# Kernel optimization log

Hardware: AMD Instinct MI355X
Metric: run time of the kernel (lower is better)

The kernel has to match this reference:

```python
import math
import jax, jax.numpy as jnp
import numpy as np

N, D, H, K = 200000, 512, 256, 64  # stocks, input_size, hidden_size, latent_size (heads)


def setup_inputs() -> dict:
    key = jax.random.key(0)
    ks = jax.random.split(key, 11)
    s = 0.02  # weight init scale
    return {
        "e": jax.random.normal(ks[0], (N, D), dtype=jnp.float32),
        "q": jax.random.normal(ks[1], (K, H), dtype=jnp.float32),  # learnable query per head
        "Wk": jax.random.normal(ks[2], (K, H, D), dtype=jnp.float32) * s,
        "bk": jax.random.normal(ks[3], (K, H), dtype=jnp.float32) * s,
        "Wv": jax.random.normal(ks[4], (K, H, D), dtype=jnp.float32) * s,
        "bv": jax.random.normal(ks[5], (K, H), dtype=jnp.float32) * s,
        "mu_w": jax.random.normal(ks[6], (H,), dtype=jnp.float32) * s,
        "mu_b": jax.random.normal(ks[7], (), dtype=jnp.float32) * s,
        "sigma_w": jax.random.normal(ks[8], (H,), dtype=jnp.float32) * s,
        "sigma_b": jax.random.normal(ks[9], (), dtype=jnp.float32) * s,
    }


def reference(e, q, Wk, bk, Wv, bv, mu_w, mu_b, sigma_w, sigma_b):
    # Per head k: scores = q . (Wk @ e_i + bk) / sqrt(H)   -> [K, N]
    # Computed as (q @ Wk) @ e.T + q.bk, avoiding the [K, N, H] key tensor.
    scale = 1.0 / math.sqrt(H)
    qWk = jnp.einsum('kh,khd->kd', q, Wk)                      # [K, D]
    scores = (jnp.einsum('kd,nd->kn', qWk, e)
              + jnp.einsum('kh,kh->k', q, bk)[:, None]) * scale  # [K, N]
    attn = jax.nn.softmax(scores, axis=-1)                     # softmax over stocks
    # h_att = attn @ (e @ Wv.T + bv); since attn sums to 1, bias term is bv exactly.
    pooled = jnp.einsum('kn,nd->kd', attn, e)                  # [K, D]
    h_multi = jnp.einsum('kd,khd->kh', pooled, Wv) + bv        # [K, H]
    mu_prior = h_multi @ mu_w + mu_b                           # [K]
    sigma_prior = jnp.exp(h_multi @ sigma_w + sigma_b)         # [K]
    return mu_prior, sigma_prior
```

## Files before the change

kernel.cpp:

```cpp
#include <hip/hip_runtime.h>
#include <math.h>
#include <stdint.h>

#define NROWS 200000
#define DDIM  512
#define HDIM  256
#define KHEADS 64
#define NB    32
#define NITER (NROWS / NB)
#define GRID  512

typedef __attribute__((ext_vector_type(8))) short bf16x8;
typedef __attribute__((ext_vector_type(4))) float f32x4;

__device__ __forceinline__ uint32_t f2bf1(float x) {
    uint32_t u = __float_as_uint(x);
    return (u + 0x7FFFu + ((u >> 16) & 1u)) >> 16;
}
__device__ __forceinline__ uint32_t pk2(float a, float b) {
    uint32_t r;
    asm("v_cvt_pk_bf16_f32 %0, %1, %2" : "=v"(r) : "v"(a), "v"(b));
    return r;
}

__global__ __launch_bounds__(256)
void prep(const float* __restrict__ q, const float* __restrict__ Wk,
          unsigned short* __restrict__ qwkb)
{
    const int k    = blockIdx.x >> 3;
    const int dq   = blockIdx.x & 7;
    const int t    = threadIdx.x;
    const int cd   = t & 63;
    const int hseg = t >> 6;
    const int d    = dq * 64 + cd;
    const float* wk = Wk + ((size_t)k << 17);
    const float* qk = q + (k << 8);
    const float* wp = wk + (hseg * 64) * 512 + d;
    const float* qp = qk + hseg * 64;
    float s0 = 0.f, s1 = 0.f, s2 = 0.f, s3 = 0.f;
    #pragma unroll 4
    for (int h = 0; h < 64; h += 4) {
        s0 = fmaf(qp[h],     wp[(h    ) * 512], s0);
        s1 = fmaf(qp[h + 1], wp[(h + 1) * 512], s1);
        s2 = fmaf(qp[h + 2], wp[(h + 2) * 512], s2);
        s3 = fmaf(qp[h + 3], wp[(h + 3) * 512], s3);
    }
    float s = (s0 + s1) + (s2 + s3);
    __shared__ float red[4][64];
    red[hseg][cd] = s;
    __syncthreads();
    if (t < 64) {
        float tot = (red[0][t] + red[1][t]) + (red[2][t] + red[3][t]);
        qwkb[(k << 9) + dq * 64 + t] = (unsigned short)f2bf1(tot * 0.0625f);
    }
}

__global__ void qbk_kernel(const float* __restrict__ q, const float* __restrict__ bk,
                           float* __restrict__ qbk)
{
    int k = threadIdx.x;
    const float4* q4 = (const float4*)(q + (k << 8));
    const float4* b4 = (const float4*)(bk + (k << 8));
    float s = 0.f;
    for (int i = 0; i < 64; ++i) {
        float4 a = q4[i], b = b4[i];
        s += a.x * b.x + a.y * b.y + a.z * b.z + a.w * b.w;
    }
    qbk[k] = s * 0.0625f;
}

__global__ __launch_bounds__(256, 2)
void fused_attn(const float* __restrict__ e,
                const unsigned short* __restrict__ qwkb,
                const float* __restrict__ qbk,
                float* __restrict__ pooled, float* __restrict__ lsum,
                float* __restrict__ parts, float* __restrict__ lparts,
                int use_parts)
{
    __shared__ char lds[65536];

    const int t    = threadIdx.x;
    const int w    = t >> 6;
    const int lane = t & 63;
    const int c    = lane & 15;
    const int Q    = lane >> 4;

    bf16x8 bq[16];
    {
        const char* qb_ = (const char*)qwkb + (w * 16 + c) * 1024 + Q * 16;
        #pragma unroll
        for (int ks = 0; ks < 16; ++ks)
            bq[ks] = *(const bf16x8*)(qb_ + ks * 64);
    }
    const float qbias = qbk[w * 16 + c];

    f32x4 acc[32];
    #pragma unroll
    for (int i = 0; i < 32; ++i) { f32x4 z = {0.f, 0.f, 0.f, 0.f}; acc[i] = z; }
    float l_part = 0.f;

    for (int b = blockIdx.x; b < NITER; b += GRID) {
        __syncthreads();
        const float4* eg = (const float4*)(e + (size_t)b * (NB * DDIM));
        #pragma unroll
        for (int i = 0; i < 4; ++i) {
            const int bb = t + i * 256;
            const int rg = bb >> 7, dg = bb & 127;
            float4 v0 = eg[(rg * 4 + 0) * 128 + dg];
            float4 v1 = eg[(rg * 4 + 1) * 128 + dg];
            float4 v2 = eg[(rg * 4 + 2) * 128 + dg];
            float4 v3 = eg[(rg * 4 + 3) * 128 + dg];
            const float* r0 = (const float*)&v0;
            const float* r1 = (const float*)&v1;
            const float* r2 = (const float*)&v2;
            const float* r3 = (const float*)&v3;
            {
                const int chA  = (rg >> 2) * 16 + (dg >> 3);
                const int lnD  = ((dg >> 1) & 3) * 16;
                const int byA  = (dg & 1) * 8;
                const int base = chA * 1024 + byA;
                const int sw   = chA & 7;
                int ln0 = (((rg & 3) * 4 + 0) + lnD) ^ sw;
                int ln1 = (((rg & 3) * 4 + 1) + lnD) ^ sw;
                int ln2 = (((rg & 3) * 4 + 2) + lnD) ^ sw;
                int ln3 = (((rg & 3) * 4 + 3) + lnD) ^ sw;
                *(uint2*)(lds + base + ln0 * 16) = make_uint2(pk2(r0[0], r0[1]), pk2(r0[2], r0[3]));
                *(uint2*)(lds + base + ln1 * 16) = make_uint2(pk2(r1[0], r1[1]), pk2(r1[2], r1[3]));
                *(uint2*)(lds + base + ln2 * 16) = make_uint2(pk2(r2[0], r2[1]), pk2(r2[2], r2[3]));
                *(uint2*)(lds + base + ln3 * 16) = make_uint2(pk2(r3[0], r3[1]), pk2(r3[2], r3[3]));
            }
            {
                const int chB  = dg >> 2;
                const int lnR  = ((rg >> 1) & 3) * 16;
                const int byB  = (rg & 1) * 8;
                const int base = 32768 + chB * 1024 + byB;
                const int sw   = chB & 7;
                #pragma unroll
                for (int i3 = 0; i3 < 4; ++i3) {
                    int ln = (((dg & 3) * 4 + i3) + lnR) ^ sw;
                    *(uint2*)(lds + base + ln * 16) =
                        make_uint2(pk2(r0[i3], r1[i3]), pk2(r2[i3], r3[i3]));
                }
            }
        }
        __syncthreads();

        f32x4 c10 = {0.f, 0.f, 0.f, 0.f};
        f32x4 c11 = {0.f, 0.f, 0.f, 0.f};
        #pragma unroll
        for (int ks = 0; ks < 16; ++ks) {
            const bf16x8 a0 = *(const bf16x8*)(lds + ks * 1024        + ((lane ^ (ks & 7)) * 16));
            const bf16x8 a1 = *(const bf16x8*)(lds + (16 + ks) * 1024 + ((lane ^ ((16 + ks) & 7)) * 16));
            c10 = __builtin_amdgcn_mfma_f32_16x16x32_bf16(a0, bq[ks], c10, 0, 0, 0);
            c11 = __builtin_amdgcn_mfma_f32_16x16x32_bf16(a1, bq[ks], c11, 0, 0, 0);
        }

        float pe0[4], pe1[4];
        #pragma unroll
        for (int r = 0; r < 4; ++r) {
            pe0[r] = __expf(c10[r] + qbias);
            pe1[r] = __expf(c11[r] + qbias);
            l_part += pe0[r] + pe1[r];
        }

        float av[8];
        #pragma unroll
        for (int j = 0; j < 8; ++j) {
            int sq = (2 * Q + (j >> 2)) & 3;
            int sl = c + (sq << 4);
            float v0 = __shfl(pe0[j & 3], sl, 64);
            float v1 = __shfl(pe1[j & 3], sl, 64);
            av[j] = (Q >= 2) ? v1 : v0;
        }
        union { uint32_t u[4]; bf16x8 v; } a2;
        #pragma unroll
        for (int d2 = 0; d2 < 4; ++d2) a2.u[d2] = pk2(av[2 * d2], av[2 * d2 + 1]);

        #pragma unroll
        for (int ntd = 0; ntd < 32; ++ntd) {
            const bf16x8 bf_ = *(const bf16x8*)(lds + 32768 + ntd * 1024 + ((lane ^ (ntd & 7)) * 16));
            acc[ntd] = __builtin_amdgcn_mfma_f32_16x16x32_bf16(a2.v, bf_, acc[ntd], 0, 0, 0);
        }
    }

    float lt = l_part;
    lt += __shfl_xor(lt, 16, 64);
    lt += __shfl_xor(lt, 32, 64);

    if (use_parts) {
        float* pp = parts + (size_t)blockIdx.x * (KHEADS * DDIM);
        #pragma unroll
        for (int ntd = 0; ntd < 32; ++ntd)
            #pragma unroll
            for (int r = 0; r < 4; ++r)
                pp[(w * 16 + Q * 4 + r) * DDIM + ntd * 16 + c] = acc[ntd][r];
        if (Q == 0) lparts[blockIdx.x * KHEADS + w * 16 + c] = lt;
    } else {
        #pragma unroll
        for (int ntd = 0; ntd < 32; ++ntd)
            #pragma unroll
            for (int r = 0; r < 4; ++r)
                atomicAdd(&pooled[(w * 16 + Q * 4 + r) * DDIM + ntd * 16 + c], acc[ntd][r]);
        if (Q == 0) atomicAdd(&lsum[w * 16 + c], lt);
    }
}

__global__ __launch_bounds__(256)
void reduce_parts(const float* __restrict__ parts, const float* __restrict__ lparts,
                  float* __restrict__ pooled, float* __restrict__ lsum)
{
    const int t   = threadIdx.x;
    const int bid = blockIdx.x;
    if (bid < 512) {
        const int o4    = t & 15;
        const int chunk = t >> 4;
        const float4* p4 = (const float4*)parts;
        const int base4 = bid * 16 + o4;
        float4 s = make_float4(0.f, 0.f, 0.f, 0.f);
        #pragma unroll 8
        for (int b = chunk * 32; b < chunk * 32 + 32; ++b) {
            float4 v = p4[b * 8192 + base4];
            s.x += v.x; s.y += v.y; s.z += v.z; s.w += v.w;
        }
        __shared__ float4 red[16][16];
        red[chunk][o4] = s;
        __syncthreads();
        if (t < 16) {
            float4 a = red[0][t];
            #pragma unroll
            for (int i = 1; i < 16; ++i) {
                float4 v = red[i][t];
                a.x += v.x; a.y += v.y; a.z += v.z; a.w += v.w;
            }
            ((float4*)pooled)[bid * 16 + t] = a;
        }
    } else {
        const int k = t & 63, chunk = t >> 6;
        float s = 0.f;
        #pragma unroll 8
        for (int b = chunk * 128; b < chunk * 128 + 128; ++b)
            s += lparts[b * 64 + k];
        __shared__ float redl[4][64];
        redl[chunk][k] = s;
        __syncthreads();
        if (t < 64) lsum[t] = (redl[0][t] + redl[1][t]) + (redl[2][t] + redl[3][t]);
    }
}

__global__ __launch_bounds__(256)
void finalize_partial(const float* __restrict__ pooled, const float* __restrict__ lsum,
                      const float* __restrict__ Wv, const float* __restrict__ bv,
                      const float* __restrict__ mu_w, const float* __restrict__ sigma_w,
                      float* __restrict__ macc, float* __restrict__ sacc)
{
    const int k  = blockIdx.x >> 3;
    const int hg = blockIdx.x & 7;
    const int t  = threadIdx.x;
    __shared__ float pn[DDIM];
    __shared__ float sm[32], ss[32];
    const float inv_l = 1.0f / lsum[k];
    pn[t]       = pooled[(k << 9) + t] * inv_l;
    pn[t + 256] = pooled[(k << 9) + t + 256] * inv_l;
    __syncthreads();
    const int hi = t >> 3, ds = t & 7;
    const int h  = hg * 32 + hi;
    const float4* wv4 = (const float4*)(Wv + ((size_t)(k * 256 + h) << 9));
    const float4* pn4 = (const float4*)pn;
    float s = 0.f;
    #pragma unroll
    for (int i = 0; i < 16; ++i) {
        float4 a  = pn4[ds + i * 8];
        float4 b_ = wv4[ds + i * 8];
        s += a.x * b_.x + a.y * b_.y + a.z * b_.z + a.w * b_.w;
    }
    s += __shfl_down(s, 4, 64);
    s += __shfl_down(s, 2, 64);
    s += __shfl_down(s, 1, 64);
    if (ds == 0) {
        float hval = s + bv[(k << 8) + h];
        sm[hi] = hval * mu_w[h];
        ss[hi] = hval * sigma_w[h];
    }
    __syncthreads();
    if (t == 0) {
        float m = 0.f, sg = 0.f;
        for (int i = 0; i < 32; ++i) { m += sm[i]; sg += ss[i]; }
        atomicAdd(&macc[k], m);
        atomicAdd(&sacc[k], sg);
    }
}

__global__ void final_out(const float* __restrict__ macc, const float* __restrict__ sacc,
                          const float* __restrict__ mu_b, const float* __restrict__ sigma_b,
                          float* __restrict__ out)
{
    int k = threadIdx.x;
    out[k]          = macc[k] + mu_b[0];
    out[KHEADS + k] = __expf(sacc[k] + sigma_b[0]);
}

extern "C" void kernel_launch(void* const* d_in, const int* in_sizes, int n_in,
                              void* d_out, int out_size, void* d_ws, size_t ws_size,
                              hipStream_t stream)
{
    const float* e       = (const float*)d_in[0];
    const float* q       = (const float*)d_in[1];
    const float* Wk      = (const float*)d_in[2];
    const float* bk      = (const float*)d_in[3];
    const float* Wv      = (const float*)d_in[4];
    const float* bv      = (const float*)d_in[5];
    const float* mu_w    = (const float*)d_in[6];
    const float* mu_b    = (const float*)d_in[7];
    const float* sigma_w = (const float*)d_in[8];
    const float* sigma_b = (const float*)d_in[9];
    float* out = (float*)d_out;

    char* wsb = (char*)d_ws;
    unsigned short* qwkb = (unsigned short*)wsb;
    float* qbk    = (float*)(wsb + 65536);
    float* pooled = (float*)(wsb + 65792);
    float* lsum   = (float*)(wsb + 196864);
    float* macc   = (float*)(wsb + 197120);
    float* sacc   = (float*)(wsb + 197376);
    float* parts  = (float*)(wsb + 197632);
    float* lparts = (float*)(wsb + 197632 + (size_t)GRID * KHEADS * DDIM * 4);
    const size_t need = 197632 + (size_t)GRID * KHEADS * DDIM * 4 + (size_t)GRID * KHEADS * 4;
    const int use_parts = (ws_size >= need) ? 1 : 0;

    if (use_parts)
        hipMemsetAsync(macc, 0, 512, stream);
    else
        hipMemsetAsync(pooled, 0, 131072 + 768, stream);

    prep<<<512, 256, 0, stream>>>(q, Wk, qwkb);
    qbk_kernel<<<1, 64, 0, stream>>>(q, bk, qbk);
    fused_attn<<<GRID, 256, 0, stream>>>(e, qwkb, qbk, pooled, lsum, parts, lparts, use_parts);
    if (use_parts)
        reduce_parts<<<513, 256, 0, stream>>>(parts, lparts, pooled, lsum);
    finalize_partial<<<512, 256, 0, stream>>>(pooled, lsum, Wv, bv, mu_w, sigma_w, macc, sacc);
    final_out<<<1, 64, 0, stream>>>(macc, sacc, mu_b, sigma_b, out);
}
```

Measured before the change: 643.3 us.

## Prefetch half of next e tile into registers and fold qbk into prep

The main attention loop now loads half of the next iteration's e tile into registers (8 float4s) right after the LDS staging barrier, so those global loads overlap the MFMA and softmax work of the current tile. Loads of e use nontemporal hints because e is streamed once. The separate qbk kernel is merged into the prep kernel as an extra block, saving one launch. The register prefetch raises VGPR pressure in a kernel already holding 32 accumulators and 16 query fragments under a 2-waves-per-SIMD launch bound, so spills are possible.

```diff
diff --git a/kernel.cpp b/kernel.cpp
--- a/kernel.cpp
+++ b/kernel.cpp
@@ -25,8 +25,24 @@
 
 __global__ __launch_bounds__(256)
 void prep(const float* __restrict__ q, const float* __restrict__ Wk,
-          unsigned short* __restrict__ qwkb)
-{
+          const float* __restrict__ bk,
+          unsigned short* __restrict__ qwkb, float* __restrict__ qbk)
+{
+    if (blockIdx.x == 512) {
+        const int k = threadIdx.x;
+        if (k < KHEADS) {
+            const float4* q4 = (const float4*)(q + (k << 8));
+            const float4* b4 = (const float4*)(bk + (k << 8));
+            float s = 0.f;
+            #pragma unroll 8
+            for (int i = 0; i < 64; ++i) {
+                float4 a = q4[i], b = b4[i];
+                s += a.x * b.x + a.y * b.y + a.z * b.z + a.w * b.w;
+            }
+            qbk[k] = s * 0.0625f;
+        }
+        return;
+    }
     const int k    = blockIdx.x >> 3;
     const int dq   = blockIdx.x & 7;
     const int t    = threadIdx.x;
@@ -55,20 +71,6 @@
     }
 }
 
-__global__ void qbk_kernel(const float* __restrict__ q, const float* __restrict__ bk,
-                           float* __restrict__ qbk)
-{
-    int k = threadIdx.x;
-    const float4* q4 = (const float4*)(q + (k << 8));
-    const float4* b4 = (const float4*)(bk + (k << 8));
-    float s = 0.f;
-    for (int i = 0; i < 64; ++i) {
-        float4 a = q4[i], b = b4[i];
-        s += a.x * b.x + a.y * b.y + a.z * b.z + a.w * b.w;
-    }
-    qbk[k] = s * 0.0625f;
-}
-
 __global__ __launch_bounds__(256, 2)
 void fused_attn(const float* __restrict__ e,
                 const unsigned short* __restrict__ qwkb,
@@ -99,51 +101,86 @@
     for (int i = 0; i < 32; ++i) { f32x4 z = {0.f, 0.f, 0.f, 0.f}; acc[i] = z; }
     float l_part = 0.f;
 
+    auto stage = [&](int i, const f32x4& v0, const f32x4& v1,
+                     const f32x4& v2, const f32x4& v3) {
+        const int bb = t + i * 256;
+        const int rg = bb >> 7, dg = bb & 127;
+        const float* r0 = (const float*)&v0;
+        const float* r1 = (const float*)&v1;
+        const float* r2 = (const float*)&v2;
+        const float* r3 = (const float*)&v3;
+        {
+            const int chA  = (rg >> 2) * 16 + (dg >> 3);
+            const int lnD  = ((dg >> 1) & 3) * 16;
+            const int byA  = (dg & 1) * 8;
+            const int base = chA * 1024 + byA;
+            const int sw   = chA & 7;
+            int ln0 = (((rg & 3) * 4 + 0) + lnD) ^ sw;
+            int ln1 = (((rg & 3) * 4 + 1) + lnD) ^ sw;
+            int ln2 = (((rg & 3) * 4 + 2) + lnD) ^ sw;
+            int ln3 = (((rg & 3) * 4 + 3) + lnD) ^ sw;
+            *(uint2*)(lds + base + ln0 * 16) = make_uint2(pk2(r0[0], r0[1]), pk2(r0[2], r0[3]));
+            *(uint2*)(lds + base + ln1 * 16) = make_uint2(pk2(r1[0], r1[1]), pk2(r1[2], r1[3]));
+            *(uint2*)(lds + base + ln2 * 16) = make_uint2(pk2(r2[0], r2[1]), pk2(r2[2], r2[3]));
+            *(uint2*)(lds + base + ln3 * 16) = make_uint2(pk2(r3[0], r3[1]), pk2(r3[2], r3[3]));
+        }
+        {
+            const int chB  = dg >> 2;
+            const int lnR  = ((rg >> 1) & 3) * 16;
+            const int byB  = (rg & 1) * 8;
+            const int base = 32768 + chB * 1024 + byB;
+            const int sw   = chB & 7;
+            #pragma unroll
+            for (int i3 = 0; i3 < 4; ++i3) {
+                int ln = (((dg & 3) * 4 + i3) + lnR) ^ sw;
+                *(uint2*)(lds + base + ln * 16) =
+                    make_uint2(pk2(r0[i3], r1[i3]), pk2(r2[i3], r3[i3]));
+            }
+        }
+    };
+
+    f32x4 pf[8];
+    {
+        const f32x4* eg = (const f32x4*)(e + (size_t)blockIdx.x * (NB * DDIM));
+        #pragma unroll
+        for (int i = 0; i < 2; ++i) {
+            const int bb = t + i * 256;
+            const int rg = bb >> 7, dg = bb & 127;
+            #pragma unroll
+            for (int r = 0; r < 4; ++r)
+                pf[i * 4 + r] = __builtin_nontemporal_load(&eg[(rg * 4 + r) * 128 + dg]);
+        }
+    }
+
     for (int b = blockIdx.x; b < NITER; b += GRID) {
         __syncthreads();
-        const float4* eg = (const float4*)(e + (size_t)b * (NB * DDIM));
-        #pragma unroll
-        for (int i = 0; i < 4; ++i) {
+        stage(0, pf[0], pf[1], pf[2], pf[3]);
+        stage(1, pf[4], pf[5], pf[6], pf[7]);
+        const f32x4* eg = (const f32x4*)(e + (size_t)b * (NB * DDIM));
+        #pragma unroll
+        for (int i = 2; i < 4; ++i) {
             const int bb = t + i * 256;
             const int rg = bb >> 7, dg = bb & 127;
-            float4 v0 = eg[(rg * 4 + 0) * 128 + dg];
-            float4 v1 = eg[(rg * 4 + 1) * 128 + dg];
-            float4 v2 = eg[(rg * 4 + 2) * 128 + dg];
-            float4 v3 = eg[(rg * 4 + 3) * 128 + dg];
-            const float* r0 = (const float*)&v0;
-            const float* r1 = (const float*)&v1;
-            const float* r2 = (const float*)&v2;
-            const float* r3 = (const float*)&v3;
-            {
-                const int chA  = (rg >> 2) * 16 + (dg >> 3);
-                const int lnD  = ((dg >> 1) & 3) * 16;
-                const int byA  = (dg & 1) * 8;
-                const int base = chA * 1024 + byA;
-                const int sw   = chA & 7;
-                int ln0 = (((rg & 3) * 4 + 0) + lnD) ^ sw;
-                int ln1 = (((rg & 3) * 4 + 1) + lnD) ^ sw;
-                int ln2 = (((rg & 3) * 4 + 2) + lnD) ^ sw;
-                int ln3 = (((rg & 3) * 4 + 3) + lnD) ^ sw;
-                *(uint2*)(lds + base + ln0 * 16) = make_uint2(pk2(r0[0], r0[1]), pk2(r0[2], r0[3]));
-                *(uint2*)(lds + base + ln1 * 16) = make_uint2(pk2(r1[0], r1[1]), pk2(r1[2], r1[3]));
-                *(uint2*)(lds + base + ln2 * 16) = make_uint2(pk2(r2[0], r2[1]), pk2(r2[2], r2[3]));
-                *(uint2*)(lds + base + ln3 * 16) = make_uint2(pk2(r3[0], r3[1]), pk2(r3[2], r3[3]));
+            f32x4 v0 = __builtin_nontemporal_load(&eg[(rg * 4 + 0) * 128 + dg]);
+            f32x4 v1 = __builtin_nontemporal_load(&eg[(rg * 4 + 1) * 128 + dg]);
+            f32x4 v2 = __builtin_nontemporal_load(&eg[(rg * 4 + 2) * 128 + dg]);
+            f32x4 v3 = __builtin_nontemporal_load(&eg[(rg * 4 + 3) * 128 + dg]);
+            stage(i, v0, v1, v2, v3);
+        }
+        __syncthreads();
+
+        const int bn = b + GRID;
+        if (bn < NITER) {
+            const f32x4* eg2 = (const f32x4*)(e + (size_t)bn * (NB * DDIM));
+            #pragma unroll
+            for (int i = 0; i < 2; ++i) {
+                const int bb = t + i * 256;
+                const int rg = bb >> 7, dg = bb & 127;
+                #pragma unroll
+                for (int r = 0; r < 4; ++r)
+                    pf[i * 4 + r] = __builtin_nontemporal_load(&eg2[(rg * 4 + r) * 128 + dg]);
             }
-            {
-                const int chB  = dg >> 2;
-                const int lnR  = ((rg >> 1) & 3) * 16;
-                const int byB  = (rg & 1) * 8;
-                const int base = 32768 + chB * 1024 + byB;
-                const int sw   = chB & 7;
-                #pragma unroll
-                for (int i3 = 0; i3 < 4; ++i3) {
-                    int ln = (((dg & 3) * 4 + i3) + lnR) ^ sw;
-                    *(uint2*)(lds + base + ln * 16) =
-                        make_uint2(pk2(r0[i3], r1[i3]), pk2(r2[i3], r3[i3]));
-                }
-            }
-        }
-        __syncthreads();
+        }
 
         f32x4 c10 = {0.f, 0.f, 0.f, 0.f};
         f32x4 c11 = {0.f, 0.f, 0.f, 0.f};
@@ -328,12 +365,11 @@
     const int use_parts = (ws_size >= need) ? 1 : 0;
 
     if (use_parts)
-        hipMemsetAsync(macc, 0, 512, stream);
+        (void)hipMemsetAsync(macc, 0, 512, stream);
     else
-        hipMemsetAsync(pooled, 0, 131072 + 768, stream);
-
-    prep<<<512, 256, 0, stream>>>(q, Wk, qwkb);
-    qbk_kernel<<<1, 64, 0, stream>>>(q, bk, qbk);
+        (void)hipMemsetAsync(pooled, 0, 131072 + 768, stream);
+
+    prep<<<513, 256, 0, stream>>>(q, Wk, bk, qwkb, qbk);
     fused_attn<<<GRID, 256, 0, stream>>>(e, qwkb, qbk, pooled, lsum, parts, lparts, use_parts);
     if (use_parts)
         reduce_parts<<<513, 256, 0, stream>>>(parts, lparts, pooled, lsum);
```

Result: slower. 724.9 us (+12.7%).
